# Optimization experiments

Measured on AMD Instinct MI355X. Metric: run time of the kernel, lower is better.

Reference implementation:

```python
import jax, jax.numpy as jnp
import numpy as np

N_NODES = 100000
N_EDGES = 600000
IN_DIM = 128
HID = 128
OUT_DIM = 24
NUM_LAYERS = 3


def setup_inputs() -> dict:
    key = jax.random.key(0)
    ks = jax.random.split(key, 12)
    x = jax.random.normal(ks[0], (N_NODES, IN_DIM), dtype=jnp.float32)
    edge_index = jax.random.randint(ks[1], (2, N_EDGES), 0, N_NODES, dtype=jnp.int32)
    def glorot(k, fan_in, fan_out):
        s = jnp.sqrt(6.0 / (fan_in + fan_out))
        return jax.random.uniform(k, (fan_in, fan_out), jnp.float32, -s, s)
    W0 = glorot(ks[2], IN_DIM, HID)
    b0 = jnp.zeros((HID,), jnp.float32)
    W1 = glorot(ks[3], HID, HID)
    b1 = jnp.zeros((HID,), jnp.float32)
    W2 = glorot(ks[4], HID, HID)
    b2 = jnp.zeros((HID,), jnp.float32)
    lin_w = glorot(ks[5], HID, OUT_DIM)
    lin_b = jnp.zeros((OUT_DIM,), jnp.float32)
    return {"x": x, "edge_index": edge_index, "W0": W0, "b0": b0,
            "W1": W1, "b1": b1, "W2": W2, "b2": b2,
            "lin_w": lin_w, "lin_b": lin_b}


def _gcn_norm(edge_index, n_nodes):
    # PyG GCNConv default: add self-loops, symmetric normalization D^-1/2 (A+I) D^-1/2
    loops = jnp.arange(n_nodes, dtype=edge_index.dtype)
    row = jnp.concatenate([edge_index[0], loops])  # source nodes (x_j)
    col = jnp.concatenate([edge_index[1], loops])  # target nodes (aggregation)
    deg = jax.ops.segment_sum(jnp.ones_like(col, dtype=jnp.float32), col,
                              num_segments=n_nodes)
    dinv = jnp.where(deg > 0, jax.lax.rsqrt(deg), 0.0)
    norm = dinv[row] * dinv[col]  # [E + N]
    return row, col, norm


def _gcn_conv(x, W, b, row, col, norm, n_nodes):
    h = x @ W                             # linear first (PyG order)
    msg = h[row] * norm[:, None]          # gather + normalize
    agg = jax.ops.segment_sum(msg, col, num_segments=n_nodes)  # scatter-add
    return agg + b


def reference(x, edge_index, W0, b0, W1, b1, W2, b2, lin_w, lin_b):
    n = x.shape[0]
    row, col, norm = _gcn_norm(edge_index, n)
    for W, b in ((W0, b0), (W1, b1), (W2, b2)):
        x = jax.nn.elu(_gcn_conv(x, W, b, row, col, norm, n))
        # dropout p=0.1 is identity in eval mode
    pooled = jnp.mean(x, axis=0)          # global_mean_pool, single graph
    out = pooled @ lin_w + lin_b          # [24]
    return out
```

## Files before the change

### kernel.cpp

```cpp
#include <hip/hip_runtime.h>
#include <math.h>

#define NN 100000
#define NE 600000
#define DIM 128
#define SEG 1024
#define NSEG 98
#define PBLK 2048
#define G0A 782
#define G0B 781
#define CNTB 2344

typedef __attribute__((ext_vector_type(8))) short short8;
typedef __attribute__((ext_vector_type(4))) float floatx4;

static __device__ __forceinline__ unsigned short f2bf(float f) {
    union { float f; unsigned u; } v; v.f = f;
    unsigned r = v.u + 0x7fffu + ((v.u >> 16) & 1u);
    return (unsigned short)(r >> 16);
}
static __device__ __forceinline__ float bflo(unsigned int p) {
    union { unsigned u; float f; } v; v.u = p << 16; return v.f;
}
static __device__ __forceinline__ float bfhi(unsigned int p) {
    union { unsigned u; float f; } v; v.u = p & 0xffff0000u; return v.f;
}

template <bool A_IS_F32>
static __device__ void gemm_tile(const void* __restrict__ Ain,
                                 const unsigned short* __restrict__ Wp,
                                 unsigned short* __restrict__ H, int n, int tb) {
    __shared__ __align__(16) unsigned short As[64][136];
    const int t = threadIdx.x;
    const int wid = t >> 6, lane = t & 63;
    const int wy = wid & 1, wx = wid >> 1;
    const int base = tb * 64;

    short8 Bf[4][4];
    {
        const short8* wp8 = (const short8*)Wp;
#pragma unroll
        for (int tt = 0; tt < 4; ++tt)
#pragma unroll
            for (int kk = 0; kk < 4; ++kk)
                Bf[tt][kk] = wp8[(((wx * 4 + tt) * 4 + kk) * 64) + lane];
    }

    if constexpr (A_IS_F32) {
        const float* A = (const float*)Ain;
#pragma unroll
        for (int it = 0; it < 8; ++it) {
            int idx = it * 256 + t;
            int row = idx >> 5, seg = idx & 31;
            int r = base + row;
            float4 v = make_float4(0.f, 0.f, 0.f, 0.f);
            if (r < n) v = ((const float4*)(A + (size_t)r * DIM))[seg];
            ushort4 o;
            o.x = f2bf(v.x); o.y = f2bf(v.y); o.z = f2bf(v.z); o.w = f2bf(v.w);
            *((ushort4*)&As[row][seg * 4]) = o;
        }
    } else {
        const unsigned short* A = (const unsigned short*)Ain;
#pragma unroll
        for (int it = 0; it < 4; ++it) {
            int idx = it * 256 + t;
            int row = idx >> 4, seg = idx & 15;
            int r = base + row;
            uint4 v = make_uint4(0, 0, 0, 0);
            if (r < n) v = ((const uint4*)(A + (size_t)r * DIM))[seg];
            *((uint4*)&As[row][seg * 8]) = v;
        }
    }
    __syncthreads();

    floatx4 acc[2][4];
#pragma unroll
    for (int rs = 0; rs < 2; ++rs)
#pragma unroll
        for (int tt = 0; tt < 4; ++tt) acc[rs][tt] = (floatx4){0.f, 0.f, 0.f, 0.f};

    const int m = lane & 15, q = lane >> 4;
#pragma unroll
    for (int rs = 0; rs < 2; ++rs) {
        const int rbase = wy * 32 + rs * 16 + m;
        short8 Af[4];
#pragma unroll
        for (int kk = 0; kk < 4; ++kk)
            Af[kk] = *((const short8*)&As[rbase][kk * 32 + q * 8]);
#pragma unroll
        for (int kk = 0; kk < 4; ++kk)
#pragma unroll
            for (int tt = 0; tt < 4; ++tt)
                acc[rs][tt] = __builtin_amdgcn_mfma_f32_16x16x32_bf16(Af[kk], Bf[tt][kk],
                                                                     acc[rs][tt], 0, 0, 0);
    }
    __syncthreads();

#pragma unroll
    for (int rs = 0; rs < 2; ++rs)
#pragma unroll
        for (int tt = 0; tt < 4; ++tt) {
            const int col = wx * 64 + tt * 16 + m;
            const int rowb = wy * 32 + rs * 16 + q * 4;
#pragma unroll
            for (int i = 0; i < 4; ++i)
                As[rowb + i][col] = f2bf(acc[rs][tt][i]);
        }
    __syncthreads();
#pragma unroll
    for (int it = 0; it < 4; ++it) {
        int idx = it * 256 + t;
        int row = idx >> 4, seg = idx & 15;
        int r = base + row;
        if (r < n)
            ((uint4*)(H + (size_t)r * DIM))[seg] = *((const uint4*)&As[row][seg * 8]);
    }
}

__global__ __launch_bounds__(256) void k_init(int* __restrict__ counts,
                                              const float* __restrict__ W0,
                                              const float* __restrict__ W1,
                                              const float* __restrict__ W2,
                                              unsigned short* __restrict__ Wp) {
    const int bid = blockIdx.x, t = threadIdx.x;
    if (bid < 99) {
        const int base = bid * 1024 + t * 4;
#pragma unroll
        for (int i = 0; i < 4; ++i)
            if (base + i < NN + 1) counts[base + i] = 0;
    } else {
        const int wb = bid - 99;
        const int which = wb >> 6;
        const float* W = which == 0 ? W0 : (which == 1 ? W1 : W2);
        unsigned short* dst = Wp + which * 16384;
        int e = (wb & 63) * 256 + t;
        int j  = e & 7;
        int L  = (e >> 3) & 63;
        int kk = (e >> 9) & 3;
        int ct = e >> 11;
        int k = kk * 32 + (L >> 4) * 8 + j;
        int c = ct * 16 + (L & 15);
        dst[e] = f2bf(W[k * DIM + c]);
    }
}

__global__ __launch_bounds__(256) void k_g0count(const float* __restrict__ x,
                                                 const unsigned short* __restrict__ Wp,
                                                 unsigned short* __restrict__ H,
                                                 const int* __restrict__ col,
                                                 int* __restrict__ counts, int n, int E) {
    if (blockIdx.x < G0A) {
        gemm_tile<true>((const void*)x, Wp, H, n, blockIdx.x);
    } else {
        int i = (blockIdx.x - G0A) * 256 + threadIdx.x;
        if (i < E) atomicAdd(&counts[col[i]], 1);
    }
}

__global__ __launch_bounds__(256) void k_scan1(int* __restrict__ data, int* __restrict__ segsum,
                                               float* __restrict__ dinv, int n) {
    __shared__ int s[256];
    const int t = threadIdx.x;
    const int base = blockIdx.x * SEG + t * 4;
    int v[4];
#pragma unroll
    for (int i = 0; i < 4; ++i) v[i] = (base + i < n) ? data[base + i] : 0;
#pragma unroll
    for (int i = 0; i < 4; ++i)
        if (base + i < n) dinv[base + i] = rsqrtf((float)v[i] + 1.0f);
    int tsum = v[0] + v[1] + v[2] + v[3];
    s[t] = tsum;
    __syncthreads();
    for (int off = 1; off < 256; off <<= 1) {
        int x = (t >= off) ? s[t - off] : 0;
        __syncthreads();
        s[t] += x;
        __syncthreads();
    }
    int run = s[t] - tsum;
#pragma unroll
    for (int i = 0; i < 4; ++i) {
        if (base + i < n) data[base + i] = run;
        run += v[i];
    }
    if (t == 255) segsum[blockIdx.x] = s[255];
}

__global__ __launch_bounds__(256) void k_scan23(int* __restrict__ offsets,
                                                const int* __restrict__ segsum,
                                                int* __restrict__ cursor, int n) {
    __shared__ int ss[NSEG];
    __shared__ int myoff_s, total_s;
    const int t = threadIdx.x;
    if (t < NSEG) ss[t] = segsum[t];
    __syncthreads();
    if (t == 0) {
        int run = 0;
#pragma unroll 7
        for (int i = 0; i < NSEG; ++i) {
            if (i == (int)blockIdx.x) myoff_s = run;
            run += ss[i];
        }
        total_s = run;
    }
    __syncthreads();
    const int so = myoff_s;
    const int base = blockIdx.x * SEG + t * 4;
#pragma unroll
    for (int i = 0; i < 4; ++i) {
        if (base + i < n) {
            int o = offsets[base + i] + so;
            offsets[base + i] = o;
            cursor[base + i] = o;
        }
    }
    if (blockIdx.x == 0 && t == 0) offsets[n] = total_s;
}

__global__ __launch_bounds__(256) void k_g0fill(const float* __restrict__ x,
                                                const unsigned short* __restrict__ Wp,
                                                unsigned short* __restrict__ H,
                                                const int* __restrict__ rows,
                                                const int* __restrict__ cols,
                                                const float* __restrict__ dinv,
                                                int* __restrict__ cursor,
                                                int2* __restrict__ adjw, int n, int E) {
    if (blockIdx.x < G0B) {
        gemm_tile<true>((const void*)x, Wp, H, n, G0A + blockIdx.x);
    } else {
        int e = (blockIdx.x - G0B) * 256 + threadIdx.x;
        if (e < E) {
            int r = rows[e];
            int c = cols[e];
            int pos = atomicAdd(&cursor[c], 1);
            adjw[pos] = make_int2(r, __float_as_int(dinv[r] * dinv[c]));
        }
    }
}

__global__ __launch_bounds__(256) void k_gemm(const unsigned short* __restrict__ A,
                                              const unsigned short* __restrict__ Wp,
                                              unsigned short* __restrict__ H, int n) {
    gemm_tile<false>((const void*)A, Wp, H, n, blockIdx.x);
}

__global__ __launch_bounds__(256) void k_agg2(const unsigned short* __restrict__ H,
                                              const int* __restrict__ offsets,
                                              const int2* __restrict__ adjw,
                                              const float* __restrict__ dinv,
                                              const float* __restrict__ b,
                                              unsigned short* __restrict__ AGG, int n) {
    const int lane = threadIdx.x & 63;
    const int qw = lane >> 4, ql = lane & 15;
    const int p = (blockIdx.x * blockDim.x + threadIdx.x) >> 6;
    const int c = p * 4 + qw;
    if (c >= n) return;
    const float4 bb0 = ((const float4*)b)[ql * 2];
    const float4 bb1 = ((const float4*)b)[ql * 2 + 1];
    float s = dinv[c];
    s = s * s;
    uint4 hv = *(const uint4*)(H + (size_t)c * DIM + ql * 8);
    float a0 = bb0.x + bflo(hv.x) * s;
    float a1 = bb0.y + bfhi(hv.x) * s;
    float a2 = bb0.z + bflo(hv.y) * s;
    float a3 = bb0.w + bfhi(hv.y) * s;
    float a4 = bb1.x + bflo(hv.z) * s;
    float a5 = bb1.y + bfhi(hv.z) * s;
    float a6 = bb1.z + bflo(hv.w) * s;
    float a7 = bb1.w + bfhi(hv.w) * s;
    int j = offsets[c];
    const int end = offsets[c + 1];
    for (; j + 1 < end; j += 2) {
        int2 e0 = adjw[j], e1 = adjw[j + 1];
        uint4 v0 = *(const uint4*)(H + (size_t)e0.x * DIM + ql * 8);
        uint4 v1 = *(const uint4*)(H + (size_t)e1.x * DIM + ql * 8);
        float w0 = __int_as_float(e0.y), w1 = __int_as_float(e1.y);
        a0 += bflo(v0.x) * w0 + bflo(v1.x) * w1;
        a1 += bfhi(v0.x) * w0 + bfhi(v1.x) * w1;
        a2 += bflo(v0.y) * w0 + bflo(v1.y) * w1;
        a3 += bfhi(v0.y) * w0 + bfhi(v1.y) * w1;
        a4 += bflo(v0.z) * w0 + bflo(v1.z) * w1;
        a5 += bfhi(v0.z) * w0 + bfhi(v1.z) * w1;
        a6 += bflo(v0.w) * w0 + bflo(v1.w) * w1;
        a7 += bfhi(v0.w) * w0 + bfhi(v1.w) * w1;
    }
    if (j < end) {
        int2 e = adjw[j];
        uint4 v = *(const uint4*)(H + (size_t)e.x * DIM + ql * 8);
        float w = __int_as_float(e.y);
        a0 += bflo(v.x) * w;
        a1 += bfhi(v.x) * w;
        a2 += bflo(v.y) * w;
        a3 += bfhi(v.y) * w;
        a4 += bflo(v.z) * w;
        a5 += bfhi(v.z) * w;
        a6 += bflo(v.w) * w;
        a7 += bfhi(v.w) * w;
    }
    a0 = a0 > 0.f ? a0 : expf(a0) - 1.f;
    a1 = a1 > 0.f ? a1 : expf(a1) - 1.f;
    a2 = a2 > 0.f ? a2 : expf(a2) - 1.f;
    a3 = a3 > 0.f ? a3 : expf(a3) - 1.f;
    a4 = a4 > 0.f ? a4 : expf(a4) - 1.f;
    a5 = a5 > 0.f ? a5 : expf(a5) - 1.f;
    a6 = a6 > 0.f ? a6 : expf(a6) - 1.f;
    a7 = a7 > 0.f ? a7 : expf(a7) - 1.f;
    uint4 outv;
    outv.x = (unsigned int)f2bf(a0) | ((unsigned int)f2bf(a1) << 16);
    outv.y = (unsigned int)f2bf(a2) | ((unsigned int)f2bf(a3) << 16);
    outv.z = (unsigned int)f2bf(a4) | ((unsigned int)f2bf(a5) << 16);
    outv.w = (unsigned int)f2bf(a6) | ((unsigned int)f2bf(a7) << 16);
    *(uint4*)(AGG + (size_t)c * DIM + ql * 8) = outv;
}

__global__ __launch_bounds__(256) void k_aggpool2(const unsigned short* __restrict__ H,
                                                  const int* __restrict__ offsets,
                                                  const int2* __restrict__ adjw,
                                                  const float* __restrict__ dinv,
                                                  const float* __restrict__ b,
                                                  float* __restrict__ partials,
                                                  float* __restrict__ out, int n) {
    if (blockIdx.x == 0 && threadIdx.x < 24) out[threadIdx.x] = 0.f;
    const int lane = threadIdx.x & 63;
    const int qw = lane >> 4, ql = lane & 15;
    const int wib = threadIdx.x >> 6;
    int p = (blockIdx.x * blockDim.x + threadIdx.x) >> 6;
    const int np = (gridDim.x * blockDim.x) >> 6;
    const int nquad = (n + 3) >> 2;
    const float4 bb0 = ((const float4*)b)[ql * 2];
    const float4 bb1 = ((const float4*)b)[ql * 2 + 1];
    float p0 = 0.f, p1 = 0.f, p2 = 0.f, p3 = 0.f, p4 = 0.f, p5 = 0.f, p6 = 0.f, p7 = 0.f;

    for (; p < nquad; p += np) {
        const int c = p * 4 + qw;
        if (c >= n) continue;
        float s = dinv[c];
        s = s * s;
        uint4 hv = *(const uint4*)(H + (size_t)c * DIM + ql * 8);
        float a0 = bb0.x + bflo(hv.x) * s;
        float a1 = bb0.y + bfhi(hv.x) * s;
        float a2 = bb0.z + bflo(hv.y) * s;
        float a3 = bb0.w + bfhi(hv.y) * s;
        float a4 = bb1.x + bflo(hv.z) * s;
        float a5 = bb1.y + bfhi(hv.z) * s;
        float a6 = bb1.z + bflo(hv.w) * s;
        float a7 = bb1.w + bfhi(hv.w) * s;
        int j = offsets[c];
        const int end = offsets[c + 1];
        for (; j + 1 < end; j += 2) {
            int2 e0 = adjw[j], e1 = adjw[j + 1];
            uint4 v0 = *(const uint4*)(H + (size_t)e0.x * DIM + ql * 8);
            uint4 v1 = *(const uint4*)(H + (size_t)e1.x * DIM + ql * 8);
            float w0 = __int_as_float(e0.y), w1 = __int_as_float(e1.y);
            a0 += bflo(v0.x) * w0 + bflo(v1.x) * w1;
            a1 += bfhi(v0.x) * w0 + bfhi(v1.x) * w1;
            a2 += bflo(v0.y) * w0 + bflo(v1.y) * w1;
            a3 += bfhi(v0.y) * w0 + bfhi(v1.y) * w1;
            a4 += bflo(v0.z) * w0 + bflo(v1.z) * w1;
            a5 += bfhi(v0.z) * w0 + bfhi(v1.z) * w1;
            a6 += bflo(v0.w) * w0 + bflo(v1.w) * w1;
            a7 += bfhi(v0.w) * w0 + bfhi(v1.w) * w1;
        }
        if (j < end) {
            int2 e = adjw[j];
            uint4 v = *(const uint4*)(H + (size_t)e.x * DIM + ql * 8);
            float w = __int_as_float(e.y);
            a0 += bflo(v.x) * w;
            a1 += bfhi(v.x) * w;
            a2 += bflo(v.y) * w;
            a3 += bfhi(v.y) * w;
            a4 += bflo(v.z) * w;
            a5 += bfhi(v.z) * w;
            a6 += bflo(v.w) * w;
            a7 += bfhi(v.w) * w;
        }
        p0 += a0 > 0.f ? a0 : expf(a0) - 1.f;
        p1 += a1 > 0.f ? a1 : expf(a1) - 1.f;
        p2 += a2 > 0.f ? a2 : expf(a2) - 1.f;
        p3 += a3 > 0.f ? a3 : expf(a3) - 1.f;
        p4 += a4 > 0.f ? a4 : expf(a4) - 1.f;
        p5 += a5 > 0.f ? a5 : expf(a5) - 1.f;
        p6 += a6 > 0.f ? a6 : expf(a6) - 1.f;
        p7 += a7 > 0.f ? a7 : expf(a7) - 1.f;
    }

    __shared__ float ps[16][DIM];
    *(float4*)&ps[wib * 4 + qw][ql * 8] = make_float4(p0, p1, p2, p3);
    *(float4*)&ps[wib * 4 + qw][ql * 8 + 4] = make_float4(p4, p5, p6, p7);
    __syncthreads();
    const int t = threadIdx.x;
    if (t < DIM) {
        float v = 0.f;
#pragma unroll
        for (int w = 0; w < 16; ++w) v += ps[w][t];
        partials[(size_t)t * PBLK + blockIdx.x] = v;
    }
}

__global__ __launch_bounds__(256) void k_pool2final(const float* __restrict__ partials,
                                                    const float* __restrict__ lw,
                                                    const float* __restrict__ lb,
                                                    float* __restrict__ out) {
    const int d = blockIdx.x;
    const float4* row = (const float4*)(partials + (size_t)d * PBLK);
    float acc = 0.f;
#pragma unroll
    for (int i = 0; i < PBLK / 4 / 256; ++i) {
        float4 v = row[i * 256 + threadIdx.x];
        acc += v.x + v.y + v.z + v.w;
    }
#pragma unroll
    for (int off = 32; off; off >>= 1) acc += __shfl_down(acc, off, 64);
    __shared__ float wsum[4];
    if ((threadIdx.x & 63) == 0) wsum[threadIdx.x >> 6] = acc;
    __syncthreads();
    if (threadIdx.x < 24) {
        float pooled_d = wsum[0] + wsum[1] + wsum[2] + wsum[3];
        float contrib = pooled_d * lw[d * 24 + threadIdx.x] * (1.0f / (float)NN);
        if (d == 0) contrib += lb[threadIdx.x];
        atomicAdd(&out[threadIdx.x], contrib);
    }
}

extern "C" void kernel_launch(void* const* d_in, const int* in_sizes, int n_in,
                              void* d_out, int out_size, void* d_ws, size_t ws_size,
                              hipStream_t stream) {
    const float* x  = (const float*)d_in[0];
    const int*   ei = (const int*)d_in[1];
    const float* W0 = (const float*)d_in[2];
    const float* b0 = (const float*)d_in[3];
    const float* W1 = (const float*)d_in[4];
    const float* b1 = (const float*)d_in[5];
    const float* W2 = (const float*)d_in[6];
    const float* b2 = (const float*)d_in[7];
    const float* lw = (const float*)d_in[8];
    const float* lb = (const float*)d_in[9];
    float* out = (float*)d_out;

    const int N = NN, E = NE;
    const int* rows = ei;
    const int* cols = ei + E;

    char* ws = (char*)d_ws;
    unsigned short* H   = (unsigned short*)ws;
    unsigned short* AGG = (unsigned short*)(ws + 25600000);
    float* dinv    = (float*)(ws + 51200000);
    int*   offsets = (int*)(ws + 51600512);
    int*   cursor  = (int*)(ws + 52000640);
    int*   segsum  = (int*)(ws + 52400640);
    int2*  adjw    = (int2*)(ws + 52401152);
    unsigned short* Wp = (unsigned short*)(ws + 57201152);
    float* partials = (float*)(ws + 57299456);

    const int agg_grid = (N + 15) / 16;
    const int gemm_grid = (N + 63) / 64;

    k_init<<<291, 256, 0, stream>>>(offsets, W0, W1, W2, Wp);
    k_g0count<<<G0A + CNTB, 256, 0, stream>>>(x, Wp, H, cols, offsets, N, E);
    k_scan1<<<NSEG, 256, 0, stream>>>(offsets, segsum, dinv, N);
    k_scan23<<<NSEG, 256, 0, stream>>>(offsets, segsum, cursor, N);
    k_g0fill<<<G0B + CNTB, 256, 0, stream>>>(x, Wp, H, rows, cols, dinv, cursor, adjw, N, E);

    k_agg2<<<agg_grid, 256, 0, stream>>>(H, offsets, adjw, dinv, b0, AGG, N);
    k_gemm<<<gemm_grid, 256, 0, stream>>>(AGG, Wp + 16384, H, N);
    k_agg2<<<agg_grid, 256, 0, stream>>>(H, offsets, adjw, dinv, b1, AGG, N);
    k_gemm<<<gemm_grid, 256, 0, stream>>>(AGG, Wp + 32768, H, N);
    k_aggpool2<<<PBLK, 256, 0, stream>>>(H, offsets, adjw, dinv, b2, partials, out, N);

    k_pool2final<<<DIM, 256, 0, stream>>>(partials, lw, lb, out);
}
```

Before: 295.5 us.

## Split layer-0 GEMM from CSR build kernels and fuse pooling into final aggregation

The first-layer GEMM is pulled out of the histogram and fill kernels into a standalone launch. The histogram now processes two edges per thread with an int2 load. The separate pool-final kernel is removed: each aggregation block projects its partial pooled sum through lin_w and atomically adds into the output, which is now zeroed in k_init. This removes one launch and the partials round trip, but gives up overlapping the GEMM with the atomic-heavy CSR construction and adds 2048×24 atomics on the output.

```diff
diff --git a/kernel.cpp b/kernel.cpp
--- a/kernel.cpp
+++ b/kernel.cpp
@@ -7,9 +7,6 @@
 #define SEG 1024
 #define NSEG 98
 #define PBLK 2048
-#define G0A 782
-#define G0B 781
-#define CNTB 2344
 
 typedef __attribute__((ext_vector_type(8))) short short8;
 typedef __attribute__((ext_vector_type(4))) float floatx4;
@@ -121,13 +118,15 @@
                                               const float* __restrict__ W0,
                                               const float* __restrict__ W1,
                                               const float* __restrict__ W2,
-                                              unsigned short* __restrict__ Wp) {
+                                              unsigned short* __restrict__ Wp,
+                                              float* __restrict__ out) {
     const int bid = blockIdx.x, t = threadIdx.x;
     if (bid < 99) {
         const int base = bid * 1024 + t * 4;
 #pragma unroll
         for (int i = 0; i < 4; ++i)
             if (base + i < NN + 1) counts[base + i] = 0;
+        if (bid == 0 && t < 24) out[t] = 0.f;
     } else {
         const int wb = bid - 99;
         const int which = wb >> 6;
@@ -144,16 +143,15 @@
     }
 }
 
-__global__ __launch_bounds__(256) void k_g0count(const float* __restrict__ x,
-                                                 const unsigned short* __restrict__ Wp,
-                                                 unsigned short* __restrict__ H,
-                                                 const int* __restrict__ col,
-                                                 int* __restrict__ counts, int n, int E) {
-    if (blockIdx.x < G0A) {
-        gemm_tile<true>((const void*)x, Wp, H, n, blockIdx.x);
-    } else {
-        int i = (blockIdx.x - G0A) * 256 + threadIdx.x;
-        if (i < E) atomicAdd(&counts[col[i]], 1);
+__global__ __launch_bounds__(256) void k_hist(const int* __restrict__ col,
+                                              int* __restrict__ counts, int E) {
+    int e = (blockIdx.x * 256 + threadIdx.x) * 2;
+    if (e + 1 < E) {
+        int2 c2 = *(const int2*)(col + e);
+        atomicAdd(&counts[c2.x], 1);
+        atomicAdd(&counts[c2.y], 1);
+    } else if (e < E) {
+        atomicAdd(&counts[col[e]], 1);
     }
 }
 
@@ -217,25 +215,24 @@
     if (blockIdx.x == 0 && t == 0) offsets[n] = total_s;
 }
 
-__global__ __launch_bounds__(256) void k_g0fill(const float* __restrict__ x,
-                                                const unsigned short* __restrict__ Wp,
-                                                unsigned short* __restrict__ H,
-                                                const int* __restrict__ rows,
-                                                const int* __restrict__ cols,
-                                                const float* __restrict__ dinv,
-                                                int* __restrict__ cursor,
-                                                int2* __restrict__ adjw, int n, int E) {
-    if (blockIdx.x < G0B) {
-        gemm_tile<true>((const void*)x, Wp, H, n, G0A + blockIdx.x);
-    } else {
-        int e = (blockIdx.x - G0B) * 256 + threadIdx.x;
-        if (e < E) {
-            int r = rows[e];
-            int c = cols[e];
-            int pos = atomicAdd(&cursor[c], 1);
-            adjw[pos] = make_int2(r, __float_as_int(dinv[r] * dinv[c]));
-        }
-    }
+__global__ __launch_bounds__(256) void k_fill(const int* __restrict__ rows,
+                                              const int* __restrict__ cols,
+                                              const float* __restrict__ dinv,
+                                              int* __restrict__ cursor,
+                                              int2* __restrict__ adjw, int E) {
+    int e = blockIdx.x * 256 + threadIdx.x;
+    if (e < E) {
+        int r = rows[e];
+        int c = cols[e];
+        int pos = atomicAdd(&cursor[c], 1);
+        adjw[pos] = make_int2(r, __float_as_int(dinv[r] * dinv[c]));
+    }
+}
+
+__global__ __launch_bounds__(256) void k_gemm0(const float* __restrict__ x,
+                                               const unsigned short* __restrict__ Wp,
+                                               unsigned short* __restrict__ H, int n) {
+    gemm_tile<true>((const void*)x, Wp, H, n, blockIdx.x);
 }
 
 __global__ __launch_bounds__(256) void k_gemm(const unsigned short* __restrict__ A,
@@ -318,9 +315,9 @@
                                                   const int2* __restrict__ adjw,
                                                   const float* __restrict__ dinv,
                                                   const float* __restrict__ b,
-                                                  float* __restrict__ partials,
+                                                  const float* __restrict__ lw,
+                                                  const float* __restrict__ lb,
                                                   float* __restrict__ out, int n) {
-    if (blockIdx.x == 0 && threadIdx.x < 24) out[threadIdx.x] = 0.f;
     const int lane = threadIdx.x & 63;
     const int qw = lane >> 4, ql = lane & 15;
     const int wib = threadIdx.x >> 6;
@@ -389,36 +386,21 @@
     *(float4*)&ps[wib * 4 + qw][ql * 8 + 4] = make_float4(p4, p5, p6, p7);
     __syncthreads();
     const int t = threadIdx.x;
+    __shared__ float pooled[DIM];
     if (t < DIM) {
         float v = 0.f;
 #pragma unroll
         for (int w = 0; w < 16; ++w) v += ps[w][t];
-        partials[(size_t)t * PBLK + blockIdx.x] = v;
-    }
-}
-
-__global__ __launch_bounds__(256) void k_pool2final(const float* __restrict__ partials,
-                                                    const float* __restrict__ lw,
-                                                    const float* __restrict__ lb,
-                                                    float* __restrict__ out) {
-    const int d = blockIdx.x;
-    const float4* row = (const float4*)(partials + (size_t)d * PBLK);
-    float acc = 0.f;
-#pragma unroll
-    for (int i = 0; i < PBLK / 4 / 256; ++i) {
-        float4 v = row[i * 256 + threadIdx.x];
-        acc += v.x + v.y + v.z + v.w;
-    }
-#pragma unroll
-    for (int off = 32; off; off >>= 1) acc += __shfl_down(acc, off, 64);
-    __shared__ float wsum[4];
-    if ((threadIdx.x & 63) == 0) wsum[threadIdx.x >> 6] = acc;
-    __syncthreads();
-    if (threadIdx.x < 24) {
-        float pooled_d = wsum[0] + wsum[1] + wsum[2] + wsum[3];
-        float contrib = pooled_d * lw[d * 24 + threadIdx.x] * (1.0f / (float)NN);
-        if (d == 0) contrib += lb[threadIdx.x];
-        atomicAdd(&out[threadIdx.x], contrib);
+        pooled[t] = v;
+    }
+    __syncthreads();
+    if (t < 24) {
+        float acc = 0.f;
+#pragma unroll 8
+        for (int d = 0; d < DIM; ++d) acc += pooled[d] * lw[d * 24 + t];
+        acc *= (1.0f / (float)NN);
+        if (blockIdx.x == 0) acc += lb[t];
+        atomicAdd(&out[t], acc);
     }
 }
 
@@ -450,22 +432,20 @@
     int*   segsum  = (int*)(ws + 52400640);
     int2*  adjw    = (int2*)(ws + 52401152);
     unsigned short* Wp = (unsigned short*)(ws + 57201152);
-    float* partials = (float*)(ws + 57299456);
 
     const int agg_grid = (N + 15) / 16;
     const int gemm_grid = (N + 63) / 64;
 
-    k_init<<<291, 256, 0, stream>>>(offsets, W0, W1, W2, Wp);
-    k_g0count<<<G0A + CNTB, 256, 0, stream>>>(x, Wp, H, cols, offsets, N, E);
+    k_init<<<291, 256, 0, stream>>>(offsets, W0, W1, W2, Wp, out);
+    k_hist<<<(E / 2 + 255) / 256, 256, 0, stream>>>(cols, offsets, E);
     k_scan1<<<NSEG, 256, 0, stream>>>(offsets, segsum, dinv, N);
     k_scan23<<<NSEG, 256, 0, stream>>>(offsets, segsum, cursor, N);
-    k_g0fill<<<G0B + CNTB, 256, 0, stream>>>(x, Wp, H, rows, cols, dinv, cursor, adjw, N, E);
+    k_fill<<<(E + 255) / 256, 256, 0, stream>>>(rows, cols, dinv, cursor, adjw, E);
+    k_gemm0<<<gemm_grid, 256, 0, stream>>>(x, Wp, H, N);
 
     k_agg2<<<agg_grid, 256, 0, stream>>>(H, offsets, adjw, dinv, b0, AGG, N);
     k_gemm<<<gemm_grid, 256, 0, stream>>>(AGG, Wp + 16384, H, N);
     k_agg2<<<agg_grid, 256, 0, stream>>>(H, offsets, adjw, dinv, b1, AGG, N);
     k_gemm<<<gemm_grid, 256, 0, stream>>>(AGG, Wp + 32768, H, N);
-    k_aggpool2<<<PBLK, 256, 0, stream>>>(H, offsets, adjw, dinv, b2, partials, out, N);
-
-    k_pool2final<<<DIM, 256, 0, stream>>>(partials, lw, lb, out);
-}
+    k_aggpool2<<<PBLK, 256, 0, stream>>>(H, offsets, adjw, dinv, b2, lw, lb, out, N);
+}
```

New measurement: 322.1 us. 1.09x slower.
